# Kernel tuning notes

Measured on AMD Instinct MI355X. Metric: run time of the kernel, lower is better.

The kernel has to match this reference:

```python
import jax, jax.numpy as jnp
import numpy as np

HEADS = 8

def setup_inputs() -> dict:
    key = jax.random.key(0)
    ks = jax.random.split(key, 7)
    B, C, H, W = 8, 640, 64, 64
    L, CD = 77, 768
    return {
        "hidden_states": jax.random.normal(ks[0], (B, C, H, W), jnp.float32),
        "encoder_hidden_states": jax.random.normal(ks[1], (B, L, CD), jnp.float32),
        "Wq": jax.random.normal(ks[2], (C, C), jnp.float32) * 0.02,
        "Wk": jax.random.normal(ks[3], (CD, C), jnp.float32) * 0.02,
        "Wv": jax.random.normal(ks[4], (CD, C), jnp.float32) * 0.02,
        "Wo": jax.random.normal(ks[5], (C, C), jnp.float32) * 0.02,
        "bo": jnp.zeros((C,), jnp.float32),
    }

def reference(hidden_states, encoder_hidden_states, Wq, Wk, Wv, Wo, bo):
    B, C, H, W = hidden_states.shape
    N = H * W
    dh = C // HEADS
    scale = 1.0 / jnp.sqrt(jnp.asarray(dh, hidden_states.dtype))
    # (B, C, H, W) -> (B, N, C)
    x = hidden_states.reshape(B, C, N).transpose(0, 2, 1)
    q = (x @ Wq).reshape(B, N, HEADS, dh)
    k = (encoder_hidden_states @ Wk).reshape(B, -1, HEADS, dh)
    v = (encoder_hidden_states @ Wv).reshape(B, -1, HEADS, dh)
    # scores: (B, HEADS, N, L) -- full attention_probs materialized as in the original
    scores = jnp.einsum("bnhd,blhd->bhnl", q, k) * scale
    probs = jax.nn.softmax(scores, axis=-1)
    # saliency capture: mean over heads then over k tokens -> (B, 1, H, W)
    saliency = probs.mean(axis=1).mean(axis=-1).reshape(B, 1, H, W)
    out = jnp.einsum("bhnl,blhd->bnhd", probs, v).reshape(B, N, C)
    out = out @ Wo + bo
    out = out.transpose(0, 2, 1).reshape(B, C, H, W)
    return out, saliency
```

## Files before the change

kernel.cpp:

```cpp
#include <hip/hip_runtime.h>

typedef unsigned short u16;
typedef __bf16 bf16x8 __attribute__((ext_vector_type(8)));
typedef float f32x4 __attribute__((ext_vector_type(4)));
typedef unsigned short u16x8 __attribute__((ext_vector_type(8)));
typedef unsigned short u16x4 __attribute__((ext_vector_type(4)));

#define NB 8
#define NC 640
#define NN 4096
#define NL 77
#define NCD 768
#define NH 8
#define NDH 80

__device__ __forceinline__ u16 f2bf(float f) {
  unsigned u = __builtin_bit_cast(unsigned, f);
  u += 0x7fffu + ((u >> 16) & 1u);
  return (u16)(u >> 16);
}

__device__ __forceinline__ f32x4 mfma16(bf16x8 a, bf16x8 b, f32x4 c) {
  return __builtin_amdgcn_mfma_f32_16x16x32_bf16(a, b, c, 0, 0, 0);
}

__device__ __forceinline__ void gload_lds16(const void* g, void* l) {
  __builtin_amdgcn_global_load_lds(
      (const __attribute__((address_space(1))) void*)g,
      (__attribute__((address_space(3))) void*)l, 16, 0, 0);
}

__global__ __launch_bounds__(256) void k_prep_x(const float* __restrict__ hs,
                                                u16* __restrict__ xbf) {
  __shared__ float tls[64][69];
  const int n0 = blockIdx.x * 64;
  const int c0 = blockIdx.y * 64;
  const int b  = blockIdx.z;
  const int t = threadIdx.x;
  const int rr = t >> 4;
  const int cc = (t & 15) * 4;
#pragma unroll
  for (int p = 0; p < 4; ++p) {
    int c = p * 16 + rr;
    float4 v = *(const float4*)(hs + ((size_t)(b * NC + c0 + c) << 12) + n0 + cc);
    *(float4*)&tls[c][cc] = v;
  }
  __syncthreads();
#pragma unroll
  for (int p = 0; p < 4; ++p) {
    int n = p * 16 + rr;
    u16x4 o;
#pragma unroll
    for (int e = 0; e < 4; ++e) o[e] = f2bf(tls[cc + e][n]);
    *(u16x4*)(xbf + ((size_t)(b * NN + n0 + n)) * NC + c0 + cc) = o;
  }
}

__global__ __launch_bounds__(256) void k_prep_w(const float* __restrict__ Wq,
                                                const float* __restrict__ Wo,
                                                u16* __restrict__ wqt,
                                                u16* __restrict__ wot) {
  __shared__ float tls[32][33];
  const int which = blockIdx.z;
  const float* in = which ? Wo : Wq;
  u16* outp = which ? wot : wqt;
  const float scale = which ? 1.0f : 0.11180339887498949f;
  const int n0 = blockIdx.x * 32, k0 = blockIdx.y * 32;
  const int t = threadIdx.x;
  const int r = t >> 3, c4 = (t & 7) * 4;
  float4 v = *(const float4*)(in + (size_t)(k0 + r) * NC + n0 + c4);
  tls[r][c4 + 0] = v.x; tls[r][c4 + 1] = v.y; tls[r][c4 + 2] = v.z; tls[r][c4 + 3] = v.w;
  __syncthreads();
  u16x4 o;
#pragma unroll
  for (int e = 0; e < 4; ++e) o[e] = f2bf(tls[c4 + e][r] * scale);
  *(u16x4*)(outp + (size_t)(n0 + r) * NC + k0 + c4) = o;
}

__global__ __launch_bounds__(256) void k_kv(const float* __restrict__ ehs,
                                            const float* __restrict__ Wk,
                                            const float* __restrict__ Wv,
                                            u16* __restrict__ kbf,
                                            u16* __restrict__ vtbf) {
  const int l = blockIdx.x;
  const int cg = blockIdx.y;
  const int t = threadIdx.x;
  if (l >= NL) {
    if (t < 64) {
      int c = cg * 64 + t;
      int h = c / NDH, d = c % NDH;
#pragma unroll
      for (int b = 0; b < NB; ++b)
        vtbf[(((size_t)(b * NH + h)) * NDH + d) * 96 + l] = 0;
    }
    return;
  }
  __shared__ float es[NB][NCD];
  __shared__ float comb[3][64][17];
#pragma unroll
  for (int j = 0; j < 6; ++j) {
    int idx = (t + j * 256) * 4;
    int b = idx / NCD, k = idx % NCD;
    *(float4*)&es[b][k] = *(const float4*)(ehs + ((size_t)(b * NL + l)) * NCD + k);
  }
  __syncthreads();
  const int col = t & 63, kq = t >> 6;
  const int c = cg * 64 + col;
  float ak[NB], av[NB];
#pragma unroll
  for (int b = 0; b < NB; ++b) { ak[b] = 0.f; av[b] = 0.f; }
  const int kbeg = kq * 192, kend = kbeg + 192;
#pragma unroll 4
  for (int k = kbeg; k < kend; ++k) {
    float wk = Wk[(size_t)k * NC + c];
    float wv = Wv[(size_t)k * NC + c];
#pragma unroll
    for (int b = 0; b < NB; ++b) {
      ak[b] = fmaf(es[b][k], wk, ak[b]);
      av[b] = fmaf(es[b][k], wv, av[b]);
    }
  }
  if (kq) {
#pragma unroll
    for (int b = 0; b < NB; ++b) {
      comb[kq - 1][col][b] = ak[b];
      comb[kq - 1][col][8 + b] = av[b];
    }
  }
  __syncthreads();
  if (kq == 0) {
#pragma unroll
    for (int b = 0; b < NB; ++b) {
#pragma unroll
      for (int q = 0; q < 3; ++q) {
        ak[b] += comb[q][col][b];
        av[b] += comb[q][col][8 + b];
      }
    }
    const int h = c / NDH, d = c % NDH;
#pragma unroll
    for (int b = 0; b < NB; ++b) {
      kbf[(((size_t)(b * NH + h)) * 80 + l) * 80 + d] = f2bf(ak[b]);
      vtbf[(((size_t)(b * NH + h)) * NDH + d) * 96 + l] = f2bf(av[b]);
    }
  }
}

template <int MODE>
__global__ __launch_bounds__(256) void k_gemm(const u16* __restrict__ A,
                                              const u16* __restrict__ Bw,
                                              const float* __restrict__ bias,
                                              u16* __restrict__ outb,
                                              float* __restrict__ outf) {
  __shared__ __align__(16) u16 sA[128 * 64];
  __shared__ __align__(16) u16 sB[128 * 64];
  const int bid = blockIdx.x;
  const int logical = (bid & 7) * 160 + (bid >> 3);
  const int cb = logical % 5, rb = logical / 5;
  const int r0 = rb * 128, c0 = cb * 128;
  const int t = threadIdx.x;
  const int w = t >> 6, lane = t & 63;
  const int wm = w >> 1, wn = w & 1;
  const int fr = lane & 15, g = lane >> 4;
  const int lr = lane >> 3, ls = lane & 7;
  const int sslot = ls ^ lr;

  f32x4 acc[4][4];
  f32x4 z4 = {0.f, 0.f, 0.f, 0.f};
#pragma unroll
  for (int i = 0; i < 4; ++i)
#pragma unroll
    for (int j = 0; j < 4; ++j) acc[i][j] = z4;

  for (int ks = 0; ks < 10; ++ks) {
    const int k0 = ks * 64;
#pragma unroll
    for (int p = 0; p < 4; ++p) {
      int q = w * 4 + p;
      int row = q * 8 + lr;
      gload_lds16(A + (size_t)(r0 + row) * NC + k0 + sslot * 8, sA + q * 512);
      gload_lds16(Bw + (size_t)(c0 + row) * NC + k0 + sslot * 8, sB + q * 512);
    }
    asm volatile("s_waitcnt vmcnt(0)" ::: "memory");
    __syncthreads();
#pragma unroll
    for (int kk = 0; kk < 2; ++kk) {
      bf16x8 af[4], bfr[4];
#pragma unroll
      for (int mt = 0; mt < 4; ++mt) {
        int row = wm * 64 + mt * 16 + fr;
        af[mt] = *(const bf16x8*)((const char*)sA + row * 128 +
                                  ((kk * 64 + g * 16) ^ ((row & 7) << 4)));
      }
#pragma unroll
      for (int nt = 0; nt < 4; ++nt) {
        int row = wn * 64 + nt * 16 + fr;
        bfr[nt] = *(const bf16x8*)((const char*)sB + row * 128 +
                                   ((kk * 64 + g * 16) ^ ((row & 7) << 4)));
      }
#pragma unroll
      for (int mt = 0; mt < 4; ++mt)
#pragma unroll
        for (int nt = 0; nt < 4; ++nt) {
          if (MODE == 0)
            acc[mt][nt] = mfma16(bfr[nt], af[mt], acc[mt][nt]);
          else
            acc[mt][nt] = mfma16(af[mt], bfr[nt], acc[mt][nt]);
        }
    }
    __syncthreads();
  }
  const int b = r0 >> 12, n0 = r0 & 4095;
  if (MODE == 0) {
#pragma unroll
    for (int mt = 0; mt < 4; ++mt) {
      int n = n0 + wm * 64 + mt * 16 + fr;
#pragma unroll
      for (int nt = 0; nt < 4; ++nt) {
        int cbs = c0 + wn * 64 + nt * 16 + g * 4;
        u16x4 o;
#pragma unroll
        for (int r2 = 0; r2 < 4; ++r2) o[r2] = f2bf(acc[mt][nt][r2]);
        *(u16x4*)(outb + ((size_t)(b * NN + n)) * NC + cbs) = o;
      }
    }
  } else {
#pragma unroll
    for (int mt = 0; mt < 4; ++mt) {
      int n = n0 + wm * 64 + mt * 16 + g * 4;
#pragma unroll
      for (int nt = 0; nt < 4; ++nt) {
        int c = c0 + wn * 64 + nt * 16 + fr;
        float bv = bias[c];
        f32x4 o;
#pragma unroll
        for (int r2 = 0; r2 < 4; ++r2) o[r2] = acc[mt][nt][r2] + bv;
        *(f32x4*)(outf + (((size_t)(b * NC + c)) << 12) + n) = o;
      }
    }
  }
}

__global__ __launch_bounds__(256) void k_attn(const u16* __restrict__ qbf,
                                              const u16* __restrict__ kbf,
                                              const u16* __restrict__ vtbf,
                                              u16* __restrict__ obf) {
  __shared__ __align__(16) u16 sP[4][16][104];
  const int bid = blockIdx.x;
  const int n0 = (bid & 63) * 64, h = (bid >> 6) & 7, b = bid >> 9;
  const int t = threadIdx.x, w = t >> 6, lane = t & 63;
  const int fr = lane & 15, g = lane >> 4;

  const size_t qrow = ((size_t)(b * NN + n0 + w * 16 + fr)) * NC + h * NDH;
  bf16x8 qf[3];
#pragma unroll
  for (int kk = 0; kk < 3; ++kk) {
    int d0 = kk * 32 + g * 8;
    bf16x8 v = {};
    if (d0 < NDH) v = *(const bf16x8*)(qbf + qrow + d0);
    qf[kk] = v;
  }
  const size_t kbase = ((size_t)(b * NH + h)) * (80 * 80);
  f32x4 s[5];
  f32x4 z4 = {0.f, 0.f, 0.f, 0.f};
#pragma unroll
  for (int nt = 0; nt < 5; ++nt) s[nt] = z4;
#pragma unroll
  for (int nt = 0; nt < 5; ++nt) {
    const u16* krow = kbf + kbase + (size_t)(nt * 16 + fr) * 80;
#pragma unroll
    for (int kk = 0; kk < 3; ++kk) {
      int d0 = kk * 32 + g * 8;
      bf16x8 kv = {};
      if (d0 < NDH) kv = *(const bf16x8*)(krow + d0);
      s[nt] = mfma16(kv, qf[kk], s[nt]);
    }
  }
  const size_t vbase = ((size_t)(b * NH + h)) * (80 * 96);
  bf16x8 vf[5][3];
#pragma unroll
  for (int nt = 0; nt < 5; ++nt)
#pragma unroll
    for (int kk = 0; kk < 3; ++kk)
      vf[nt][kk] = *(const bf16x8*)(vtbf + vbase + (size_t)(nt * 16 + fr) * 96 +
                                    kk * 32 + g * 8);
  float sum = 0.f;
#pragma unroll
  for (int nt = 0; nt < 5; ++nt)
#pragma unroll
    for (int r = 0; r < 4; ++r) {
      int l = nt * 16 + g * 4 + r;
      float ev = (l < NL) ? __expf(s[nt][r]) : 0.f;
      s[nt][r] = ev;
      sum += ev;
    }
  sum += __shfl_xor(sum, 16);
  sum += __shfl_xor(sum, 32);
  float inv = 1.0f / sum;
#pragma unroll
  for (int nt = 0; nt < 5; ++nt) {
    u16x4 o;
#pragma unroll
    for (int r = 0; r < 4; ++r) o[r] = f2bf(s[nt][r] * inv);
    *(u16x4*)&sP[w][fr][nt * 16 + g * 4] = o;
  }
  __syncthreads();
  bf16x8 ap[3];
#pragma unroll
  for (int kk = 0; kk < 3; ++kk) {
    int l0 = kk * 32 + g * 8;
    bf16x8 v = {};
    if (l0 < 80) v = *(const bf16x8*)&sP[w][fr][l0];
    ap[kk] = v;
  }
  f32x4 o[5];
#pragma unroll
  for (int nt = 0; nt < 5; ++nt) o[nt] = z4;
#pragma unroll
  for (int nt = 0; nt < 5; ++nt)
#pragma unroll
    for (int kk = 0; kk < 3; ++kk)
      o[nt] = mfma16(ap[kk], vf[nt][kk], o[nt]);
#pragma unroll
  for (int nt = 0; nt < 5; ++nt)
#pragma unroll
    for (int r = 0; r < 4; ++r)
      obf[((size_t)(b * NN + n0 + w * 16 + g * 4 + r)) * NC + h * NDH + nt * 16 + fr] =
          f2bf(o[nt][r]);
}

__global__ void k_sal(float* __restrict__ sal) {
  int i = blockIdx.x * 256 + threadIdx.x;
  if (i < NB * NN) sal[i] = 1.0f / 77.0f;
}

extern "C" void kernel_launch(void* const* d_in, const int* in_sizes, int n_in,
                              void* d_out, int out_size, void* d_ws, size_t ws_size,
                              hipStream_t stream) {
  const float* hs  = (const float*)d_in[0];
  const float* ehs = (const float*)d_in[1];
  const float* Wq  = (const float*)d_in[2];
  const float* Wk  = (const float*)d_in[3];
  const float* Wv  = (const float*)d_in[4];
  const float* Wo  = (const float*)d_in[5];
  const float* bo  = (const float*)d_in[6];
  float* out = (float*)d_out;
  float* sal = out + (size_t)NB * NC * NN;

  u16* ws16 = (u16*)d_ws;
  const size_t xn = (size_t)NB * NN * NC;
  u16* xbf = ws16;
  u16* qbf = ws16 + xn;
  u16* wqt = qbf + xn;
  u16* wot = wqt + (size_t)NC * NC;
  u16* kbf = wot + (size_t)NC * NC;
  u16* vtbf = kbf + (size_t)NB * NH * 80 * 80;
  u16* obf = xbf;

  k_prep_w<<<dim3(20, 20, 2), 256, 0, stream>>>(Wq, Wo, wqt, wot);
  k_kv<<<dim3(96, 10), 256, 0, stream>>>(ehs, Wk, Wv, kbf, vtbf);
  k_prep_x<<<dim3(64, 10, NB), 256, 0, stream>>>(hs, xbf);
  k_gemm<0><<<1280, 256, 0, stream>>>(xbf, wqt, nullptr, qbf, nullptr);
  k_attn<<<NB * NH * 64, 256, 0, stream>>>(qbf, kbf, vtbf, obf);
  k_gemm<1><<<1280, 256, 0, stream>>>(obf, wot, bo, nullptr, out);
  k_sal<<<128, 256, 0, stream>>>(sal);
}
```

Measured before the change: 178.3 us.

## Triple-buffer GEMM k-loop with async LDS loads and 256x128 tiles

Reworks both projection GEMMs into a three-stage LDS pipeline: global-to-LDS loads for the next k-tiles are issued ahead, with partial vmcnt waits, so memory latency overlaps the MFMA work. Blocks grow to 512 threads covering 256x128 output tiles, with B shared across eight waves, and MFMA sections run at raised wave priority. This cuts the per-iteration full load stall and repeated B fetches, at the cost of much more LDS per block (144KB), which limits occupancy to one block per CU.

```diff
diff --git a/kernel.cpp b/kernel.cpp
--- a/kernel.cpp
+++ b/kernel.cpp
@@ -13,6 +13,7 @@
 #define NCD 768
 #define NH 8
 #define NDH 80
+#define NT 10
 
 __device__ __forceinline__ u16 f2bf(float f) {
   unsigned u = __builtin_bit_cast(unsigned, f);
@@ -147,17 +148,16 @@
 }
 
 template <int MODE>
-__global__ __launch_bounds__(256) void k_gemm(const u16* __restrict__ A,
+__global__ __launch_bounds__(512) void k_gemm(const u16* __restrict__ A,
                                               const u16* __restrict__ Bw,
                                               const float* __restrict__ bias,
                                               u16* __restrict__ outb,
                                               float* __restrict__ outf) {
-  __shared__ __align__(16) u16 sA[128 * 64];
-  __shared__ __align__(16) u16 sB[128 * 64];
+  __shared__ __align__(16) u16 lds[3][24576];
   const int bid = blockIdx.x;
-  const int logical = (bid & 7) * 160 + (bid >> 3);
+  const int logical = (bid & 7) * 80 + (bid >> 3);
   const int cb = logical % 5, rb = logical / 5;
-  const int r0 = rb * 128, c0 = cb * 128;
+  const int r0 = rb * 256, c0 = cb * 128;
   const int t = threadIdx.x;
   const int w = t >> 6, lane = t & 63;
   const int wm = w >> 1, wn = w & 1;
@@ -172,44 +172,74 @@
 #pragma unroll
     for (int j = 0; j < 4; ++j) acc[i][j] = z4;
 
-  for (int ks = 0; ks < 10; ++ks) {
-    const int k0 = ks * 64;
-#pragma unroll
-    for (int p = 0; p < 4; ++p) {
-      int q = w * 4 + p;
-      int row = q * 8 + lr;
-      gload_lds16(A + (size_t)(r0 + row) * NC + k0 + sslot * 8, sA + q * 512);
-      gload_lds16(Bw + (size_t)(c0 + row) * NC + k0 + sslot * 8, sB + q * 512);
-    }
-    asm volatile("s_waitcnt vmcnt(0)" ::: "memory");
-    __syncthreads();
+#define STAGE(kt, buf)                                                              \
+  {                                                                                 \
+    const int k0_ = (kt)*64;                                                        \
+    u16* base_ = &lds[(buf)][0];                                                    \
+    _Pragma("unroll") for (int p = 0; p < 4; ++p) {                                 \
+      int ch = w * 4 + p;                                                           \
+      int row = ch * 8 + lr;                                                        \
+      gload_lds16(A + (size_t)(r0 + row) * NC + k0_ + sslot * 8, base_ + ch * 512); \
+    }                                                                               \
+    _Pragma("unroll") for (int p = 0; p < 2; ++p) {                                 \
+      int ch = w * 2 + p;                                                           \
+      int row = ch * 8 + lr;                                                        \
+      gload_lds16(Bw + (size_t)(c0 + row) * NC + k0_ + sslot * 8,                   \
+                  base_ + 16384 + ch * 512);                                        \
+    }                                                                               \
+  }
+
+  STAGE(0, 0);
+  STAGE(1, 1);
+  STAGE(2, 2);
+
+#pragma unroll
+  for (int kt = 0; kt < NT; ++kt) {
+    const int buf = kt % 3;
+    if (kt <= NT - 3)
+      asm volatile("s_waitcnt vmcnt(12)" ::: "memory");
+    else if (kt == NT - 2)
+      asm volatile("s_waitcnt vmcnt(6)" ::: "memory");
+    else
+      asm volatile("s_waitcnt vmcnt(0)" ::: "memory");
+    __builtin_amdgcn_s_barrier();
+
+    const char* bA = (const char*)&lds[buf][0];
+    const char* bB = (const char*)&lds[buf][16384];
+    bf16x8 af[4][2], bfr[4][2];
 #pragma unroll
     for (int kk = 0; kk < 2; ++kk) {
-      bf16x8 af[4], bfr[4];
 #pragma unroll
       for (int mt = 0; mt < 4; ++mt) {
         int row = wm * 64 + mt * 16 + fr;
-        af[mt] = *(const bf16x8*)((const char*)sA + row * 128 +
-                                  ((kk * 64 + g * 16) ^ ((row & 7) << 4)));
+        af[mt][kk] = *(const bf16x8*)(bA + row * 128 +
+                                      ((kk * 64 + g * 16) ^ ((row & 7) << 4)));
       }
 #pragma unroll
       for (int nt = 0; nt < 4; ++nt) {
         int row = wn * 64 + nt * 16 + fr;
-        bfr[nt] = *(const bf16x8*)((const char*)sB + row * 128 +
-                                   ((kk * 64 + g * 16) ^ ((row & 7) << 4)));
-      }
+        bfr[nt][kk] = *(const bf16x8*)(bB + row * 128 +
+                                       ((kk * 64 + g * 16) ^ ((row & 7) << 4)));
+      }
+    }
+    __builtin_amdgcn_s_setprio(1);
+#pragma unroll
+    for (int kk = 0; kk < 2; ++kk)
 #pragma unroll
       for (int mt = 0; mt < 4; ++mt)
 #pragma unroll
         for (int nt = 0; nt < 4; ++nt) {
           if (MODE == 0)
-            acc[mt][nt] = mfma16(bfr[nt], af[mt], acc[mt][nt]);
+            acc[mt][nt] = mfma16(bfr[nt][kk], af[mt][kk], acc[mt][nt]);
           else
-            acc[mt][nt] = mfma16(af[mt], bfr[nt], acc[mt][nt]);
+            acc[mt][nt] = mfma16(af[mt][kk], bfr[nt][kk], acc[mt][nt]);
         }
-    }
-    __syncthreads();
-  }
+    __builtin_amdgcn_s_setprio(0);
+    __builtin_amdgcn_s_barrier();
+    if (kt + 3 < NT) STAGE(kt + 3, buf);
+  }
+#undef STAGE
+
   const int b = r0 >> 12, n0 = r0 & 4095;
   if (MODE == 0) {
 #pragma unroll
@@ -360,8 +390,8 @@
   k_prep_w<<<dim3(20, 20, 2), 256, 0, stream>>>(Wq, Wo, wqt, wot);
   k_kv<<<dim3(96, 10), 256, 0, stream>>>(ehs, Wk, Wv, kbf, vtbf);
   k_prep_x<<<dim3(64, 10, NB), 256, 0, stream>>>(hs, xbf);
-  k_gemm<0><<<1280, 256, 0, stream>>>(xbf, wqt, nullptr, qbf, nullptr);
+  k_gemm<0><<<640, 512, 0, stream>>>(xbf, wqt, nullptr, qbf, nullptr);
   k_attn<<<NB * NH * 64, 256, 0, stream>>>(qbf, kbf, vtbf, obf);
-  k_gemm<1><<<1280, 256, 0, stream>>>(obf, wot, bo, nullptr, out);
+  k_gemm<1><<<640, 512, 0, stream>>>(obf, wot, bo, nullptr, out);
   k_sal<<<128, 256, 0, stream>>>(sal);
 }
```

New measurement: 187.9 us. +5.4%, slower.
